# Kernel tuning notes

Hardware: AMD Instinct MI355X
Metric: run time of the kernel (lower is better)

The kernel has to match this reference:

```python
import jax, jax.numpy as jnp
import numpy as np

B, N, K = 8, 4096, 16
C_IN = 3
MLP = (64, 64, 128)


def _init_conv(key, c_out, c_in):
    kw, kb = jax.random.split(key)
    bound = 1.0 / np.sqrt(c_in)
    W = jax.random.uniform(kw, (c_out, c_in), jnp.float32, -bound, bound)
    b = jax.random.uniform(kb, (c_out,), jnp.float32, -bound, bound)
    return W, b


def setup_inputs() -> dict:
    key = jax.random.key(0)
    k0, k1, k2, k3 = jax.random.split(key, 4)
    xyz = jax.random.normal(k0, (B, C_IN, N), jnp.float32)
    W0, b0 = _init_conv(k1, MLP[0], C_IN)
    W1, b1 = _init_conv(k2, MLP[1], MLP[0])
    W2, b2 = _init_conv(k3, MLP[2], MLP[1])
    return {"xyz": xyz, "W0": W0, "b0": b0, "W1": W1, "b1": b1, "W2": W2, "b2": b2}


def reference(xyz, W0, b0, W1, b1, W2, b2):
    # xyz: [B, 3, N] -> pts: [B, N, 3]
    pts = jnp.transpose(xyz, (0, 2, 1))
    # KNN: squared pairwise distances [B, N, N]
    sq = jnp.sum(pts * pts, axis=-1)  # [B, N]
    d2 = sq[:, :, None] + sq[:, None, :] - 2.0 * jnp.einsum('bnc,bmc->bnm', pts, pts)
    _, idx = jax.lax.top_k(-d2, K)  # [B, N, K] indices of K nearest (incl. self)
    # gather neighbor coords: [B, N, K, 3]
    grouped = jax.vmap(lambda p, i: p[i])(pts, idx)
    # center-relative coordinates
    rel = grouped - pts[:, :, None, :]  # [B, N, K, 3]
    # three 1x1 conv (= per-point linear) + ReLU layers
    h = jax.nn.relu(jnp.einsum('bnkc,oc->bnko', rel, W0) + b0)
    h = jax.nn.relu(jnp.einsum('bnkc,oc->bnko', h, W1) + b1)
    h = jax.nn.relu(jnp.einsum('bnkc,oc->bnko', h, W2) + b2)
    # max over K neighbors -> [B, N, D'] -> [B, D', N]
    out = jnp.max(h, axis=2)
    return jnp.transpose(out, (0, 2, 1))
```

## Files before the change

kernel.cpp:

```cpp
#include <hip/hip_runtime.h>
#include <cstddef>

#define NB   8
#define NPTS 4096
#define KNN  16
#define FCAP 64
#define QB   32

typedef _Float16 h2 __attribute__((ext_vector_type(2)));
typedef _Float16 h8 __attribute__((ext_vector_type(8)));
typedef float    f4 __attribute__((ext_vector_type(4)));
typedef float    f16f __attribute__((ext_vector_type(16)));

static __device__ __forceinline__ h2 pk2(float a, float b) {
    return __builtin_bit_cast(h2, __builtin_amdgcn_cvt_pkrtz(a, b));
}
static __device__ __forceinline__ unsigned bch(h2 v) {
    return __builtin_bit_cast(unsigned, v);
}

#if __has_builtin(__builtin_amdgcn_fmed3f)
static __device__ __forceinline__ float MED3(float a, float b, float c) {
    return __builtin_amdgcn_fmed3f(a, b, c);
}
#else
static __device__ __forceinline__ float MED3(float a, float b, float c) {
    return fmaxf(fminf(a, b), fminf(fmaxf(a, b), c));
}
#endif

static __device__ __forceinline__ float dist2(float4 Q, float4 p) {
    float dot = fmaf(Q.z, p.z, fmaf(Q.y, p.y, Q.x * p.x));
    return fmaf(-2.0f, dot, Q.w + p.w);
}

__global__ __launch_bounds__(1024) void prep_kernel(const float* __restrict__ xyz,
                                                    float4* __restrict__ pts4,
                                                    uint2* __restrict__ pm16,
                                                    unsigned* __restrict__ mx) {
    __shared__ float wred[32];
    int b = blockIdx.x, tid = threadIdx.x;
    const float* base = xyz + (size_t)b * 3 * NPTS;
    float lm = 0.0f, ls = 0.0f;
    for (int j = tid; j < NPTS; j += 1024) {
        float x = base[j];
        float y = base[NPTS + j];
        float z = base[2 * NPTS + j];
        float sq = fmaf(z, z, fmaf(y, y, x * x));
        pts4[(size_t)b * NPTS + j] = make_float4(x, y, z, sq);
        h2 lo = { (_Float16)x, (_Float16)y };
        h2 hi = { (_Float16)z, (_Float16)sq };
        pm16[(size_t)b * NPTS + j] = make_uint2(bch(lo), bch(hi));
        lm = fmaxf(lm, fmaxf(fabsf(x), fmaxf(fabsf(y), fabsf(z))));
        ls = fmaxf(ls, sq);
    }
#pragma unroll
    for (int o = 32; o; o >>= 1) {
        lm = fmaxf(lm, __shfl_xor(lm, o));
        ls = fmaxf(ls, __shfl_xor(ls, o));
    }
    int wave = tid >> 6, lane = tid & 63;
    if (lane == 0) { wred[wave] = lm; wred[16 + wave] = ls; }
    __syncthreads();
    if (tid == 0) {
        float m = wred[0], s = wred[16];
#pragma unroll
        for (int i = 1; i < 16; ++i) { m = fmaxf(m, wred[i]); s = fmaxf(s, wred[16 + i]); }
        mx[b * 2 + 0] = __builtin_bit_cast(unsigned, m);
        mx[b * 2 + 1] = __builtin_bit_cast(unsigned, s);
    }
}

__global__ __launch_bounds__(512, 8) void knn_kernel(const float4* __restrict__ pts4,
                                                     const uint2* __restrict__ pm16,
                                                     const unsigned* __restrict__ mx,
                                                     int* __restrict__ idxout) {
    __shared__ char  sbuf[8192];
    __shared__ float fdist[FCAP * QB];
    __shared__ float tauv[QB];
    __shared__ int   qcnt[QB];

    float*    partials = (float*)sbuf;
    unsigned* fidx     = (unsigned*)sbuf;

    int tid = threadIdx.x;
    int b   = blockIdx.y;
    const float4* pb  = pts4 + (size_t)b * NPTS;
    const uint2*  pmb = pm16 + (size_t)b * NPTS;

    int wave = tid >> 6, lane = tid & 63;
    int c   = wave;
    int col = lane & 31;
    int hl  = lane >> 5;
    int q   = col;
    int nq  = blockIdx.x * QB + q;
    int cbase = c * 512;

    float4 qf = pb[nq];
    float uxf = -2.0f * qf.x, uyf = -2.0f * qf.y, uzf = -2.0f * qf.z;
    _Float16 uxh = (_Float16)uxf, uyh = (_Float16)uyf, uzh = (_Float16)uzf;
    _Float16 uxl = (_Float16)(uxf - (float)uxh);
    _Float16 uyl = (_Float16)(uyf - (float)uyh);
    _Float16 uzl = (_Float16)(uzf - (float)uzh);
    uint4 bu = {0u, 0u, 0u, 0u};
    if (hl == 0) {
        h2 b01 = {uxh, uyh}, b23 = {uzh, (_Float16)1.0f};
        h2 b45 = {uxl, uyl}, b67 = {uzl, (_Float16)0.0f};
        bu.x = bch(b01); bu.y = bch(b23); bu.z = bch(b45); bu.w = bch(b67);
    }
    h8 bq = __builtin_bit_cast(h8, bu);

    {
        float c0 = __builtin_inff(), c1 = c0, c2 = c0, c3 = c0;
#pragma unroll 2
        for (int t = 0; t < 16; ++t) {
            uint4 au = {0u, 0u, 0u, 0u};
            if (hl == 0) {
                uint2 pd = pmb[cbase + t * 32 + col];
                au.x = pd.x; au.y = pd.y; au.z = pd.x; au.w = pd.y;
            }
            f16f d = __builtin_amdgcn_mfma_f32_32x32x16_f16(
                __builtin_bit_cast(h8, au), bq, (f16f)0.0f, 0, 0, 0);
            float a0 = fminf(d[0], d[1]),   a1 = fminf(d[2], d[3]);
            float a2 = fminf(d[4], d[5]),   a3 = fminf(d[6], d[7]);
            float a4 = fminf(d[8], d[9]),   a5 = fminf(d[10], d[11]);
            float a6 = fminf(d[12], d[13]), a7 = fminf(d[14], d[15]);
            float b0 = fminf(a0, a1), b1 = fminf(a2, a3);
            float b2 = fminf(a4, a5), b3 = fminf(a6, a7);
            float rmin = fminf(fminf(b0, b1), fminf(b2, b3));
            float p0 = c0, p1 = c1, p2 = c2;
            c0 = fminf(p0, rmin);
            c1 = MED3(rmin, p0, c1);
            c2 = MED3(rmin, p1, c2);
            c3 = MED3(rmin, p2, c3);
        }
        int sb = (c * 2 + hl) * 4;
        partials[(sb + 0) * QB + q] = c0;
        partials[(sb + 1) * QB + q] = c1;
        partials[(sb + 2) * QB + q] = c2;
        partials[(sb + 3) * QB + q] = c3;
    }
    __syncthreads();

    if (tid < 4 * QB) {
        int qq = tid & (QB - 1), k = tid >> 5;
        float mb[16];
#pragma unroll
        for (int j = 0; j < 16; ++j) mb[j] = __builtin_inff();
        for (int s = 0; s < 16; ++s) {
            float v = partials[(k * 16 + s) * QB + qq];
            float prev = mb[0];
            mb[0] = fminf(mb[0], v);
#pragma unroll
            for (int i = 1; i < 16; ++i) {
                float cur = mb[i];
                mb[i] = MED3(v, prev, cur);
                prev = cur;
            }
        }
#pragma unroll
        for (int j = 0; j < 16; ++j) partials[(k * 16 + j) * QB + qq] = mb[j];
    }
    __syncthreads();

    if (tid < QB) {
        float mb[16];
#pragma unroll
        for (int j = 0; j < 16; ++j) mb[j] = __builtin_inff();
        for (int k = 0; k < 4; ++k) {
            for (int j = 0; j < 16; ++j) {
                float v = partials[(k * 16 + j) * QB + tid];
                if (v >= mb[15]) break;
                float prev = mb[0];
                mb[0] = fminf(mb[0], v);
#pragma unroll
                for (int i = 1; i < 16; ++i) {
                    float cur = mb[i];
                    mb[i] = MED3(v, prev, cur);
                    prev = cur;
                }
            }
        }
        float4 q2 = pb[blockIdx.x * QB + tid];
        float sumq = fabsf(q2.x) + fabsf(q2.y) + fabsf(q2.z);
        float qn   = sqrtf(q2.w);
        float pmax = __builtin_bit_cast(float, mx[b * 2 + 0]);
        float smax = __builtin_bit_cast(float, mx[b * 2 + 1]);
        const float r11c = 4.8828125e-4f;
        float tau = mb[15];
        float E0  = smax * r11c + 2.0f * sumq * pmax * r11c + 1.0e-3f;
        float rad2 = fmaxf(tau + 2.0f * E0 + q2.w, 0.0f);
        float R   = qn + sqrtf(rad2);
        float Eq  = (R * R + 2.0f * sumq * R) * r11c + 6.0e-4f;
        Eq = fminf(Eq, E0);
        tauv[tid] = tau + 2.0f * Eq;
        qcnt[tid] = 0;
    }
    __syncthreads();

    {
        float tc = tauv[q];
#pragma unroll 1
        for (int t = 0; t < 16; ++t) {
            uint4 au = {0u, 0u, 0u, 0u};
            if (hl == 0) {
                uint2 pd = pmb[cbase + t * 32 + col];
                au.x = pd.x; au.y = pd.y; au.z = pd.x; au.w = pd.y;
            }
            f16f d = __builtin_amdgcn_mfma_f32_32x32x16_f16(
                __builtin_bit_cast(h8, au), bq, (f16f)0.0f, 0, 0, 0);
            unsigned m = 0u;
#pragma unroll
            for (int r = 0; r < 16; ++r) m |= (d[r] <= tc) ? (1u << r) : 0u;
            if (m) {
                int pos = atomicAdd(&qcnt[q], __popc(m));
                while (m) {
                    int r = __ffs(m) - 1;
                    m &= m - 1;
                    if (pos < FCAP)
                        fidx[pos * QB + q] =
                            (unsigned)(cbase + t * 32 + (r & 3) + 8 * (r >> 2) + 4 * hl);
                    ++pos;
                }
            }
        }
    }
    __syncthreads();

    for (int e = tid; e < FCAP * QB; e += 512) {
        int j = e >> 5, qq = e & (QB - 1);
        int nc = qcnt[qq]; nc = nc > FCAP ? FCAP : nc;
        if (j < nc) {
            float4 Qf = pb[blockIdx.x * QB + qq];
            fdist[e] = dist2(Qf, pb[fidx[e]]);
        }
    }
    __syncthreads();

    if (tid < QB) {
        int nqf = blockIdx.x * QB + tid;
        float4 Qf = pb[nqf];
        float bd[16]; int bi[16];
#pragma unroll
        for (int j = 0; j < 16; ++j) { bd[j] = __builtin_inff(); bi[j] = 0; }
        int cnt = qcnt[tid];
        if (cnt <= FCAP) {
            for (int j = 0; j < cnt; ++j) {
                float x  = fdist[j * QB + tid];
                int   xi = (int)fidx[j * QB + tid];
                if (x < bd[15] || (x == bd[15] && xi < bi[15])) {
#pragma unroll
                    for (int t = 0; t < 16; ++t) {
                        bool cc = (x < bd[t]) || (x == bd[t] && xi < bi[t]);
                        float nd = cc ? x  : bd[t];
                        int   ni = cc ? xi : bi[t];
                        float od = cc ? bd[t] : x;
                        int   oi = cc ? bi[t] : xi;
                        bd[t] = nd; bi[t] = ni; x = od; xi = oi;
                    }
                }
            }
        } else {
            for (int m = 0; m < NPTS; ++m) {
                float x = dist2(Qf, pb[m]);
                int  xi = m;
                if (x < bd[15] || (x == bd[15] && xi < bi[15])) {
#pragma unroll
                    for (int t = 0; t < 16; ++t) {
                        bool cc = (x < bd[t]) || (x == bd[t] && xi < bi[t]);
                        float nd = cc ? x  : bd[t];
                        int   ni = cc ? xi : bi[t];
                        float od = cc ? bd[t] : x;
                        int   oi = cc ? bi[t] : xi;
                        bd[t] = nd; bi[t] = ni; x = od; xi = oi;
                    }
                }
            }
        }
        int* op = idxout + ((size_t)b * NPTS + nqf) * KNN;
#pragma unroll
        for (int j = 0; j < 16; ++j) op[j] = bi[j];
    }
}

__global__ __launch_bounds__(256, 2) void mlp_kernel(
    const float4* __restrict__ pts4, const int* __restrict__ idxin,
    const float* __restrict__ W0, const float* __restrict__ b0,
    const float* __restrict__ W1, const float* __restrict__ b1,
    const float* __restrict__ W2, const float* __restrict__ b2,
    float* __restrict__ out) {

    int tid  = threadIdx.x;
    int wave = tid >> 6, lane = tid & 63;
    int g = lane >> 4, i = lane & 15;

    h2 w0x[8], w0y[8], w0z[8], w0b[8];
#pragma unroll
    for (int s = 0; s < 2; ++s)
#pragma unroll
        for (int v = 0; v < 4; ++v) {
            int c0 = 32 * s + 8 * g + 2 * v;
            w0x[s * 4 + v] = pk2(W0[c0 * 3 + 0], W0[c0 * 3 + 3]);
            w0y[s * 4 + v] = pk2(W0[c0 * 3 + 1], W0[c0 * 3 + 4]);
            w0z[s * 4 + v] = pk2(W0[c0 * 3 + 2], W0[c0 * 3 + 5]);
            w0b[s * 4 + v] = pk2(b0[c0], b0[c0 + 1]);
        }
    h2 b1p[8];
#pragma unroll
    for (int s = 0; s < 2; ++s)
#pragma unroll
        for (int v = 0; v < 4; ++v) {
            int c0 = 32 * s + 16 * (v >> 1) + 4 * g + 2 * (v & 1);
            b1p[s * 4 + v] = pk2(b1[c0], b1[c0 + 1]);
        }
    h8 wf1[4][2];
#pragma unroll
    for (int t = 0; t < 4; ++t)
#pragma unroll
        for (int s = 0; s < 2; ++s) {
            const float* p = W1 + (16 * t + i) * 64 + 32 * s + 8 * g;
            h8 f;
#pragma unroll
            for (int j = 0; j < 8; ++j) f[j] = (_Float16)p[j];
            wf1[t][s] = f;
        }
    h8 wf2[8][2];
#pragma unroll
    for (int t = 0; t < 8; ++t)
#pragma unroll
        for (int s = 0; s < 2; ++s) {
            const float* p = W2 + (16 * t + i) * 64;
            h8 f;
#pragma unroll
            for (int j = 0; j < 8; ++j) {
                int vc = 32 * s + 16 * (j >> 2) + 4 * g + (j & 3);
                f[j] = (_Float16)p[vc];
            }
            wf2[t][s] = f;
        }

    int gw = blockIdx.x * 4 + wave;
    int b  = gw >> 8;
    int n0 = (gw & 255) * 16;

    const float4* pb = pts4 + (size_t)b * NPTS;
    float4 q = pb[n0 + i];
    const int* ip = idxin + ((size_t)b * NPTS + n0 + i) * KNN;

    float mx[8][4];
#pragma unroll
    for (int t = 0; t < 8; ++t)
#pragma unroll
        for (int r = 0; r < 4; ++r) mx[t][r] = -3.4e38f;

    for (int it = 0; it < KNN; ++it) {
        int mi = ip[it];
        float4 p = pb[mi];
        float rx = p.x - q.x, ry = p.y - q.y, rz = p.z - q.z;
        h2 rxx = pk2(rx, rx), ryy = pk2(ry, ry), rzz = pk2(rz, rz);

        h8 h0f[2];
#pragma unroll
        for (int s = 0; s < 2; ++s)
#pragma unroll
            for (int v = 0; v < 4; ++v) {
                h2 hh = __builtin_elementwise_fma(w0z[s * 4 + v], rzz,
                         __builtin_elementwise_fma(w0y[s * 4 + v], ryy,
                          __builtin_elementwise_fma(w0x[s * 4 + v], rxx, w0b[s * 4 + v])));
                hh = __builtin_elementwise_max(hh, (h2)(_Float16)0.0f);
                h0f[s][2 * v]     = hh.x;
                h0f[s][2 * v + 1] = hh.y;
            }

        f4 d1[4];
#pragma unroll
        for (int t = 0; t < 4; ++t) {
            d1[t] = (f4)0.0f;
#pragma unroll
            for (int s = 0; s < 2; ++s)
                d1[t] = __builtin_amdgcn_mfma_f32_16x16x32_f16(wf1[t][s], h0f[s], d1[t], 0, 0, 0);
        }

        h8 h1f[2];
#pragma unroll
        for (int s = 0; s < 2; ++s)
#pragma unroll
            for (int v = 0; v < 4; ++v) {
                int t = 2 * s + (v >> 1), r0 = 2 * (v & 1);
                h2 w = pk2(d1[t][r0], d1[t][r0 + 1]);
                w = w + b1p[s * 4 + v];
                w = __builtin_elementwise_max(w, (h2)(_Float16)0.0f);
                h1f[s][2 * v]     = w.x;
                h1f[s][2 * v + 1] = w.y;
            }

#pragma unroll
        for (int t = 0; t < 8; ++t) {
            f4 d2 = (f4)0.0f;
#pragma unroll
            for (int s = 0; s < 2; ++s)
                d2 = __builtin_amdgcn_mfma_f32_16x16x32_f16(wf2[t][s], h1f[s], d2, 0, 0, 0);
#pragma unroll
            for (int r = 0; r < 4; ++r) mx[t][r] = fmaxf(mx[t][r], d2[r]);
        }
    }

    size_t ob = (size_t)b * 128 * NPTS + n0 + i;
#pragma unroll
    for (int t = 0; t < 8; ++t)
#pragma unroll
        for (int r = 0; r < 4; ++r) {
            int chn = 16 * t + 4 * g + r;
            float v = fmaxf(mx[t][r] + b2[chn], 0.0f);
            out[ob + (size_t)chn * NPTS] = v;
        }
}

extern "C" void kernel_launch(void* const* d_in, const int* in_sizes, int n_in,
                              void* d_out, int out_size, void* d_ws, size_t ws_size,
                              hipStream_t stream) {
    (void)in_sizes; (void)n_in; (void)out_size; (void)ws_size;
    const float* xyz = (const float*)d_in[0];
    const float* W0  = (const float*)d_in[1];
    const float* b0  = (const float*)d_in[2];
    const float* W1  = (const float*)d_in[3];
    const float* b1  = (const float*)d_in[4];
    const float* W2  = (const float*)d_in[5];
    const float* b2  = (const float*)d_in[6];
    float* out = (float*)d_out;

    char* ws = (char*)d_ws;
    float4*   pts4 = (float4*)ws;
    int*      idxb = (int*)(ws + (512 << 10));
    uint2*    pm16 = (uint2*)(ws + (512 << 10) + (2 << 20));
    unsigned* mxb  = (unsigned*)(ws + (512 << 10) + (2 << 20) + (256 << 10));

    prep_kernel<<<dim3(NB), dim3(1024), 0, stream>>>(xyz, pts4, pm16, mxb);
    knn_kernel<<<dim3(NPTS / QB, NB), dim3(512), 0, stream>>>(pts4, pm16, mxb, idxb);
    mlp_kernel<<<dim3(512), dim3(256), 0, stream>>>(
        pts4, idxb, W0, b0, W1, b1, W2, b2, out);
}
```

Before: 97.12 us.

## Halve KNN block size and give each wave two interleaved MFMA chains

The KNN kernel now runs with 256 threads (4 waves) per block instead of 512. Each wave scans 1024 candidate points, using two independent MFMA distance tiles per iteration that feed two separate top-4 partial trackers, so the partials layout stays the same. The per-tile row minimum now uses three-input min trees, which shortens the reduction chain. This trades per-block parallelism for instruction-level parallelism and fewer threads per block. The candidate-filtering pass becomes twice as long per wave, which may add serial latency.

```diff
diff --git a/kernel.cpp b/kernel.cpp
--- a/kernel.cpp
+++ b/kernel.cpp
@@ -28,6 +28,9 @@
     return fmaxf(fminf(a, b), fminf(fmaxf(a, b), c));
 }
 #endif
+static __device__ __forceinline__ float MIN3(float a, float b, float c) {
+    return fminf(fminf(a, b), c);
+}
 
 static __device__ __forceinline__ float dist2(float4 Q, float4 p) {
     float dot = fmaf(Q.z, p.z, fmaf(Q.y, p.y, Q.x * p.x));
@@ -71,7 +74,7 @@
     }
 }
 
-__global__ __launch_bounds__(512, 8) void knn_kernel(const float4* __restrict__ pts4,
+__global__ __launch_bounds__(256, 6) void knn_kernel(const float4* __restrict__ pts4,
                                                      const uint2* __restrict__ pm16,
                                                      const unsigned* __restrict__ mx,
                                                      int* __restrict__ idxout) {
@@ -89,12 +92,11 @@
     const uint2*  pmb = pm16 + (size_t)b * NPTS;
 
     int wave = tid >> 6, lane = tid & 63;
-    int c   = wave;
     int col = lane & 31;
     int hl  = lane >> 5;
     int q   = col;
     int nq  = blockIdx.x * QB + q;
-    int cbase = c * 512;
+    int cb  = wave * 1024;
 
     float4 qf = pb[nq];
     float uxf = -2.0f * qf.x, uyf = -2.0f * qf.y, uzf = -2.0f * qf.z;
@@ -111,34 +113,62 @@
     h8 bq = __builtin_bit_cast(h8, bu);
 
     {
-        float c0 = __builtin_inff(), c1 = c0, c2 = c0, c3 = c0;
-#pragma unroll 2
+        float a0 = __builtin_inff(), a1 = a0, a2 = a0, a3 = a0;
+        float c0 = a0, c1 = a0, c2 = a0, c3 = a0;
+#pragma unroll 1
         for (int t = 0; t < 16; ++t) {
-            uint4 au = {0u, 0u, 0u, 0u};
+            uint4 auA = {0u, 0u, 0u, 0u}, auB = {0u, 0u, 0u, 0u};
             if (hl == 0) {
-                uint2 pd = pmb[cbase + t * 32 + col];
-                au.x = pd.x; au.y = pd.y; au.z = pd.x; au.w = pd.y;
-            }
-            f16f d = __builtin_amdgcn_mfma_f32_32x32x16_f16(
-                __builtin_bit_cast(h8, au), bq, (f16f)0.0f, 0, 0, 0);
-            float a0 = fminf(d[0], d[1]),   a1 = fminf(d[2], d[3]);
-            float a2 = fminf(d[4], d[5]),   a3 = fminf(d[6], d[7]);
-            float a4 = fminf(d[8], d[9]),   a5 = fminf(d[10], d[11]);
-            float a6 = fminf(d[12], d[13]), a7 = fminf(d[14], d[15]);
-            float b0 = fminf(a0, a1), b1 = fminf(a2, a3);
-            float b2 = fminf(a4, a5), b3 = fminf(a6, a7);
-            float rmin = fminf(fminf(b0, b1), fminf(b2, b3));
-            float p0 = c0, p1 = c1, p2 = c2;
-            c0 = fminf(p0, rmin);
-            c1 = MED3(rmin, p0, c1);
-            c2 = MED3(rmin, p1, c2);
-            c3 = MED3(rmin, p2, c3);
-        }
-        int sb = (c * 2 + hl) * 4;
-        partials[(sb + 0) * QB + q] = c0;
-        partials[(sb + 1) * QB + q] = c1;
-        partials[(sb + 2) * QB + q] = c2;
-        partials[(sb + 3) * QB + q] = c3;
+                uint2 pdA = pmb[cb + t * 32 + col];
+                uint2 pdB = pmb[cb + 512 + t * 32 + col];
+                auA.x = pdA.x; auA.y = pdA.y; auA.z = pdA.x; auA.w = pdA.y;
+                auB.x = pdB.x; auB.y = pdB.y; auB.z = pdB.x; auB.w = pdB.y;
+            }
+            f16f dA = __builtin_amdgcn_mfma_f32_32x32x16_f16(
+                __builtin_bit_cast(h8, auA), bq, (f16f)0.0f, 0, 0, 0);
+            f16f dB = __builtin_amdgcn_mfma_f32_32x32x16_f16(
+                __builtin_bit_cast(h8, auB), bq, (f16f)0.0f, 0, 0, 0);
+            {
+                float v0 = MIN3(dA[0], dA[1], dA[2]);
+                float v1 = MIN3(dA[3], dA[4], dA[5]);
+                float v2 = MIN3(dA[6], dA[7], dA[8]);
+                float v3 = MIN3(dA[9], dA[10], dA[11]);
+                float v4 = MIN3(dA[12], dA[13], dA[14]);
+                float w0 = MIN3(v0, v1, v2);
+                float w1 = MIN3(v3, v4, dA[15]);
+                float rmin = fminf(w0, w1);
+                float p0 = a0, p1 = a1, p2 = a2;
+                a0 = fminf(p0, rmin);
+                a1 = MED3(rmin, p0, a1);
+                a2 = MED3(rmin, p1, a2);
+                a3 = MED3(rmin, p2, a3);
+            }
+            {
+                float v0 = MIN3(dB[0], dB[1], dB[2]);
+                float v1 = MIN3(dB[3], dB[4], dB[5]);
+                float v2 = MIN3(dB[6], dB[7], dB[8]);
+                float v3 = MIN3(dB[9], dB[10], dB[11]);
+                float v4 = MIN3(dB[12], dB[13], dB[14]);
+                float w0 = MIN3(v0, v1, v2);
+                float w1 = MIN3(v3, v4, dB[15]);
+                float rmin = fminf(w0, w1);
+                float p0 = c0, p1 = c1, p2 = c2;
+                c0 = fminf(p0, rmin);
+                c1 = MED3(rmin, p0, c1);
+                c2 = MED3(rmin, p1, c2);
+                c3 = MED3(rmin, p2, c3);
+            }
+        }
+        int g0 = ((wave * 2 + 0) * 2 + hl) * 4;
+        int g1 = ((wave * 2 + 1) * 2 + hl) * 4;
+        partials[(g0 + 0) * QB + q] = a0;
+        partials[(g0 + 1) * QB + q] = a1;
+        partials[(g0 + 2) * QB + q] = a2;
+        partials[(g0 + 3) * QB + q] = a3;
+        partials[(g1 + 0) * QB + q] = c0;
+        partials[(g1 + 1) * QB + q] = c1;
+        partials[(g1 + 2) * QB + q] = c2;
+        partials[(g1 + 3) * QB + q] = c3;
     }
     __syncthreads();
 
@@ -201,10 +231,10 @@
     {
         float tc = tauv[q];
 #pragma unroll 1
-        for (int t = 0; t < 16; ++t) {
+        for (int t = 0; t < 32; ++t) {
             uint4 au = {0u, 0u, 0u, 0u};
             if (hl == 0) {
-                uint2 pd = pmb[cbase + t * 32 + col];
+                uint2 pd = pmb[cb + t * 32 + col];
                 au.x = pd.x; au.y = pd.y; au.z = pd.x; au.w = pd.y;
             }
             f16f d = __builtin_amdgcn_mfma_f32_32x32x16_f16(
@@ -219,7 +249,7 @@
                     m &= m - 1;
                     if (pos < FCAP)
                         fidx[pos * QB + q] =
-                            (unsigned)(cbase + t * 32 + (r & 3) + 8 * (r >> 2) + 4 * hl);
+                            (unsigned)(cb + t * 32 + (r & 3) + 8 * (r >> 2) + 4 * hl);
                     ++pos;
                 }
             }
@@ -227,7 +257,7 @@
     }
     __syncthreads();
 
-    for (int e = tid; e < FCAP * QB; e += 512) {
+    for (int e = tid; e < FCAP * QB; e += 256) {
         int j = e >> 5, qq = e & (QB - 1);
         int nc = qcnt[qq]; nc = nc > FCAP ? FCAP : nc;
         if (j < nc) {
@@ -436,7 +466,7 @@
     unsigned* mxb  = (unsigned*)(ws + (512 << 10) + (2 << 20) + (256 << 10));
 
     prep_kernel<<<dim3(NB), dim3(1024), 0, stream>>>(xyz, pts4, pm16, mxb);
-    knn_kernel<<<dim3(NPTS / QB, NB), dim3(512), 0, stream>>>(pts4, pm16, mxb, idxb);
+    knn_kernel<<<dim3(NPTS / QB, NB), dim3(256), 0, stream>>>(pts4, pm16, mxb, idxb);
     mlp_kernel<<<dim3(512), dim3(256), 0, stream>>>(
         pts4, idxb, W0, b0, W1, b1, W2, b2, out);
 }
```

After: 95.73 us. Within noise of the previous version (-1.4%).
